# Optimization experiments

Hardware: AMD Instinct MI355X
Metric: run time of the kernel (lower is better)

Reference implementation:

```python
import jax, jax.numpy as jnp
import numpy as np

N, E, H, W, K = 16, 128, 128, 128, 8  # batch, num_experts, height, width, top-k


def setup_inputs() -> dict:
    key = jax.random.key(0)
    k1, k2, k3 = jax.random.split(key, 3)
    return {
        "x": jax.random.normal(k1, (N, E, H, W), dtype=jnp.float32),        # unused by forward math (kept for signature fidelity)
        "experts": jax.random.normal(k2, (N, E, H, W), dtype=jnp.float32),  # per-expert output maps
        "gate_w": jax.random.normal(k3, (E, E), dtype=jnp.float32) * 0.05,  # 1x1 gating projection (out, in)
        "gate_b": jnp.zeros((E,), dtype=jnp.float32),
    }


def reference(x, experts, gate_w, gate_b):
    # Gate: 1x1 conv over the expert-channel dim -> per-pixel routing logits, then softmax.
    logits = jnp.einsum('nehw,fe->nfhw', experts, gate_w) + gate_b[None, :, None, None]
    routing_weights = jax.nn.softmax(logits, axis=1)  # [N, E, H, W]

    # SMoERouting: per-pixel top-k expert selection, gather expert values, scale by gate weight.
    rw_t = jnp.transpose(routing_weights, (0, 2, 3, 1))       # [N, H, W, E]
    top_vals, top_idx = jax.lax.top_k(rw_t, K)                # [N, H, W, K]
    experts_t = jnp.transpose(experts, (0, 2, 3, 1))          # [N, H, W, E]
    gathered = jnp.take_along_axis(experts_t, top_idx, axis=-1)  # irregular gather [N, H, W, K]
    selected = gathered * top_vals
    return jnp.transpose(selected, (0, 3, 1, 2))              # [N, K, H, W]
```

## Files before the change

kernel.cpp:

```cpp
#include <hip/hip_runtime.h>
#include <math.h>

#define NB 16
#define NE 128
#define NK 8
#define HW 16384
#define NPIX (NB * HW)

__device__ float g_gwT[NE * NE];

__global__ __launch_bounds__(256) void cvt_gw_kernel(const float* __restrict__ gate_w) {
    int i = blockIdx.x * 256 + threadIdx.x;
    if (i < NE * NE) {
        int e = i >> 7;
        int f = i & 127;
        g_gwT[i] = gate_w[f * NE + e];
    }
}

__global__ __launch_bounds__(256) void moe_kernel(const float* __restrict__ experts,
                                                  const float* __restrict__ gate_b,
                                                  float* __restrict__ out) {
    const int p  = blockIdx.x * 256 + threadIdx.x;
    const int n  = p >> 14;
    const int hw = p & (HW - 1);

    const float* xp = experts + ((size_t)n * NE * HW + hw);

    float acc[NE];
#pragma unroll
    for (int f = 0; f < NE; ++f) acc[f] = 0.0f;

    for (int e = 0; e < NE; ++e) {
        float xe = xp[(size_t)e * HW];
        const float* gw = &g_gwT[e * NE];
#pragma unroll
        for (int f = 0; f < NE; ++f) {
            acc[f] = fmaf(gw[f], xe, acc[f]);
        }
    }

#pragma unroll
    for (int f = 0; f < NE; ++f) acc[f] = acc[f] + gate_b[f];

    float m = acc[0];
#pragma unroll
    for (int f = 1; f < NE; ++f) m = fmaxf(m, acc[f]);

#pragma unroll
    for (int f = 0; f < NE; ++f) {
        acc[f] = (float)exp((double)(acc[f] - m));
    }

    float s = acc[0];
#pragma unroll
    for (int f = 1; f < NE; ++f) s = s + acc[f];

#pragma unroll
    for (int f = 0; f < NE; ++f) acc[f] = acc[f] / s;

    float t_v[NK];
    int   t_i[NK];
#pragma unroll
    for (int i = 0; i < NK; ++i) { t_v[i] = -1.0f; t_i[i] = 0; }

#pragma unroll
    for (int f = 0; f < NE; ++f) {
        float v  = acc[f];
        int   ix = f;
#pragma unroll
        for (int i = 0; i < NK; ++i) {
            bool gt = v > t_v[i];
            float tv = t_v[i]; int ti = t_i[i];
            t_v[i] = gt ? v  : tv;
            t_i[i] = gt ? ix : ti;
            v      = gt ? tv : v;
            ix     = gt ? ti : ix;
        }
    }

    float* op = out + ((size_t)n * NK * HW + hw);
#pragma unroll
    for (int k = 0; k < NK; ++k) {
        float xv = xp[(size_t)t_i[k] * HW];
        op[(size_t)k * HW] = t_v[k] * xv;
    }
}

extern "C" void kernel_launch(void* const* d_in, const int* in_sizes, int n_in,
                              void* d_out, int out_size, void* d_ws, size_t ws_size,
                              hipStream_t stream) {
    const float* experts = (const float*)d_in[1];
    const float* gate_w  = (const float*)d_in[2];
    const float* gate_b  = (const float*)d_in[3];
    float* out = (float*)d_out;

    hipLaunchKernelGGL(cvt_gw_kernel, dim3((NE * NE + 255) / 256), dim3(256), 0, stream, gate_w);
    hipLaunchKernelGGL(moe_kernel, dim3(NPIX / 256), dim3(256), 0, stream, experts, gate_b, out);
}
```

Before: 287.2 us.

## Use packed FP32 FMA with scalar gate weights and prefetch expert loads

Replaces the scalar per-output FMA loop with v_pk_fma_f32 inline asm that takes two gate weights at a time from scalar registers, which halves the VALU instruction count of the 128x128 projection. Expert values are loaded four channels ahead to hide global memory latency, and launch bounds now request two blocks per CU. Inline asm with an "s" constraint relies on the weights being wave-uniform and may cost extra SGPR moves, and the occupancy hint could cause register spills.

```diff
diff --git a/kernel.cpp b/kernel.cpp
--- a/kernel.cpp
+++ b/kernel.cpp
@@ -6,6 +6,8 @@
 #define NK 8
 #define HW 16384
 #define NPIX (NB * HW)
+
+typedef float v2f __attribute__((ext_vector_type(2)));
 
 __device__ float g_gwT[NE * NE];
 
@@ -18,46 +20,86 @@
     }
 }
 
-__global__ __launch_bounds__(256) void moe_kernel(const float* __restrict__ experts,
-                                                  const float* __restrict__ gate_b,
-                                                  float* __restrict__ out) {
+#define E_STEP(EIDX, XV)                                                \
+    {                                                                   \
+        v2f xb; xb.x = (XV); xb.y = (XV);                               \
+        const v2f* g2 = (const v2f*)&g_gwT[(size_t)(EIDX) * NE];        \
+        _Pragma("unroll")                                               \
+        for (int j = 0; j < NE / 2; ++j) {                              \
+            asm("v_pk_fma_f32 %0, %2, %1, %0"                           \
+                : "+v"(acc[j])                                          \
+                : "v"(xb), "s"(g2[j]));                                 \
+        }                                                               \
+    }
+
+__global__ __launch_bounds__(256, 2) void moe_kernel(const float* __restrict__ experts,
+                                                     const float* __restrict__ gate_b,
+                                                     float* __restrict__ out) {
     const int p  = blockIdx.x * 256 + threadIdx.x;
     const int n  = p >> 14;
     const int hw = p & (HW - 1);
 
     const float* xp = experts + ((size_t)n * NE * HW + hw);
 
-    float acc[NE];
+    v2f acc[NE / 2];
 #pragma unroll
-    for (int f = 0; f < NE; ++f) acc[f] = 0.0f;
+    for (int j = 0; j < NE / 2; ++j) acc[j] = (v2f){0.0f, 0.0f};
 
-    for (int e = 0; e < NE; ++e) {
-        float xe = xp[(size_t)e * HW];
-        const float* gw = &g_gwT[e * NE];
+    float xc0 = xp[0 * (size_t)HW];
+    float xc1 = xp[1 * (size_t)HW];
+    float xc2 = xp[2 * (size_t)HW];
+    float xc3 = xp[3 * (size_t)HW];
+
+    int e = 0;
+    for (; e < NE - 4; e += 4) {
+        float nx0 = xp[(size_t)(e + 4) * HW];
+        float nx1 = xp[(size_t)(e + 5) * HW];
+        float nx2 = xp[(size_t)(e + 6) * HW];
+        float nx3 = xp[(size_t)(e + 7) * HW];
+        E_STEP(e + 0, xc0);
+        E_STEP(e + 1, xc1);
+        E_STEP(e + 2, xc2);
+        E_STEP(e + 3, xc3);
+        xc0 = nx0; xc1 = nx1; xc2 = nx2; xc3 = nx3;
+    }
+    E_STEP(e + 0, xc0);
+    E_STEP(e + 1, xc1);
+    E_STEP(e + 2, xc2);
+    E_STEP(e + 3, xc3);
+
 #pragma unroll
-        for (int f = 0; f < NE; ++f) {
-            acc[f] = fmaf(gw[f], xe, acc[f]);
-        }
+    for (int j = 0; j < NE / 2; ++j) {
+        acc[j].x = acc[j].x + gate_b[2 * j];
+        acc[j].y = acc[j].y + gate_b[2 * j + 1];
+    }
+
+    float m = acc[0].x;
+    m = fmaxf(m, acc[0].y);
+#pragma unroll
+    for (int j = 1; j < NE / 2; ++j) {
+        m = fmaxf(m, acc[j].x);
+        m = fmaxf(m, acc[j].y);
     }
 
 #pragma unroll
-    for (int f = 0; f < NE; ++f) acc[f] = acc[f] + gate_b[f];
+    for (int j = 0; j < NE / 2; ++j) {
+        acc[j].x = (float)exp((double)(acc[j].x - m));
+        acc[j].y = (float)exp((double)(acc[j].y - m));
+    }
 
-    float m = acc[0];
+    float s = acc[0].x;
+    s = s + acc[0].y;
 #pragma unroll
-    for (int f = 1; f < NE; ++f) m = fmaxf(m, acc[f]);
+    for (int j = 1; j < NE / 2; ++j) {
+        s = s + acc[j].x;
+        s = s + acc[j].y;
+    }
 
 #pragma unroll
-    for (int f = 0; f < NE; ++f) {
-        acc[f] = (float)exp((double)(acc[f] - m));
+    for (int j = 0; j < NE / 2; ++j) {
+        acc[j].x = acc[j].x / s;
+        acc[j].y = acc[j].y / s;
     }
-
-    float s = acc[0];
-#pragma unroll
-    for (int f = 1; f < NE; ++f) s = s + acc[f];
-
-#pragma unroll
-    for (int f = 0; f < NE; ++f) acc[f] = acc[f] / s;
 
     float t_v[NK];
     int   t_i[NK];
@@ -65,17 +107,20 @@
     for (int i = 0; i < NK; ++i) { t_v[i] = -1.0f; t_i[i] = 0; }
 
 #pragma unroll
-    for (int f = 0; f < NE; ++f) {
-        float v  = acc[f];
-        int   ix = f;
+    for (int j = 0; j < NE / 2; ++j) {
 #pragma unroll
-        for (int i = 0; i < NK; ++i) {
-            bool gt = v > t_v[i];
-            float tv = t_v[i]; int ti = t_i[i];
-            t_v[i] = gt ? v  : tv;
-            t_i[i] = gt ? ix : ti;
-            v      = gt ? tv : v;
-            ix     = gt ? ti : ix;
+        for (int h = 0; h < 2; ++h) {
+            float v  = h ? acc[j].y : acc[j].x;
+            int   ix = 2 * j + h;
+#pragma unroll
+            for (int i = 0; i < NK; ++i) {
+                bool gt = v > t_v[i];
+                float tv = t_v[i]; int ti = t_i[i];
+                t_v[i] = gt ? v  : tv;
+                t_i[i] = gt ? ix : ti;
+                v      = gt ? tv : v;
+                ix     = gt ? ti : ix;
+            }
         }
     }
 
```

Result: slower. 802.0 us (+179.2%).

## Double-buffer expert channel loads into LDS via async global_load_lds

Applied to the files above, without the earlier changes.

The expert values are now staged into shared memory in chunks of 16 channels using the direct global-to-LDS load builtin. A double buffer prefetches the next chunk while the current one feeds the per-pixel gate FMAs, with a barrier after each chunk. This aims to hide global load latency in the gating matmul loop. In exchange it adds 16 KB of LDS per block and a block-wide barrier per chunk. Synchronisation on the async loads relies only on __syncthreads and there is no explicit wait on the LDS-load counter.

```diff
diff --git a/kernel.cpp b/kernel.cpp
--- a/kernel.cpp
+++ b/kernel.cpp
@@ -6,6 +6,9 @@
 #define NK 8
 #define HW 16384
 #define NPIX (NB * HW)
+
+#define CH 16
+#define NCHUNK (NE / CH)
 
 __device__ float g_gwT[NE * NE];
 
@@ -21,24 +24,52 @@
 __global__ __launch_bounds__(256) void moe_kernel(const float* __restrict__ experts,
                                                   const float* __restrict__ gate_b,
                                                   float* __restrict__ out) {
-    const int p  = blockIdx.x * 256 + threadIdx.x;
-    const int n  = p >> 14;
-    const int hw = p & (HW - 1);
+    const int tid = threadIdx.x;
+    const int wv  = tid >> 6;
+    const int p   = blockIdx.x * 256 + tid;
+    const int n   = p >> 14;
+    const int hw  = p & (HW - 1);
 
-    const float* xp = experts + ((size_t)n * NE * HW + hw);
+    const float* xp    = experts + ((size_t)n * NE * HW + hw);
+    const float* xbase = experts + ((size_t)n * NE * HW + ((size_t)blockIdx.x * 256 & (HW - 1)));
+
+    __shared__ float xs[2][CH][256];
+
+#define STAGE(c, b)                                                                   \
+    {                                                                                 \
+        const float* gsrc = xbase + (size_t)(c) * CH * HW;                            \
+        _Pragma("unroll")                                                             \
+        for (int i = 0; i < CH; ++i) {                                                \
+            __builtin_amdgcn_global_load_lds(                                         \
+                (const __attribute__((address_space(1))) void*)(gsrc + (size_t)i * HW + tid), \
+                (__attribute__((address_space(3))) void*)&xs[b][i][wv * 64],          \
+                4, 0, 0);                                                             \
+        }                                                                             \
+    }
 
     float acc[NE];
 #pragma unroll
     for (int f = 0; f < NE; ++f) acc[f] = 0.0f;
 
-    for (int e = 0; e < NE; ++e) {
-        float xe = xp[(size_t)e * HW];
-        const float* gw = &g_gwT[e * NE];
+    STAGE(0, 0);
+    __syncthreads();
+
+    for (int c = 0; c < NCHUNK; ++c) {
+        const int cur = c & 1;
+        if (c + 1 < NCHUNK) STAGE(c + 1, cur ^ 1);
+
 #pragma unroll
-        for (int f = 0; f < NE; ++f) {
-            acc[f] = fmaf(gw[f], xe, acc[f]);
+        for (int i = 0; i < CH; ++i) {
+            float xe = xs[cur][i][tid];
+            const float* gw = &g_gwT[(size_t)(c * CH + i) * NE];
+#pragma unroll
+            for (int f = 0; f < NE; ++f) {
+                acc[f] = fmaf(gw[f], xe, acc[f]);
+            }
         }
+        __syncthreads();
     }
+#undef STAGE
 
 #pragma unroll
     for (int f = 0; f < NE; ++f) acc[f] = acc[f] + gate_b[f];
```

New measurement: 584.2 us. +103.4%, slower.

## Stage gate weights in LDS and prefetch expert inputs in groups of eight

Applied to the files above, without the earlier changes.

Each block copies the transposed 128x128 gate matrix into shared memory and then reads it with float4 broadcast loads instead of scalar global loads. The expert loads are software-pipelined: the next group of eight channel values is fetched while the current group is accumulated. This targets global-memory and scalar load latency in the gating matmul. It costs 64KB of LDS per block, which limits occupancy, adds extra registers on top of the 128 accumulators, and every block repeats the copy.

```diff
diff --git a/kernel.cpp b/kernel.cpp
--- a/kernel.cpp
+++ b/kernel.cpp
@@ -21,22 +21,55 @@
 __global__ __launch_bounds__(256) void moe_kernel(const float* __restrict__ experts,
                                                   const float* __restrict__ gate_b,
                                                   float* __restrict__ out) {
-    const int p  = blockIdx.x * 256 + threadIdx.x;
-    const int n  = p >> 14;
-    const int hw = p & (HW - 1);
+    const int tid = threadIdx.x;
+    const int p   = blockIdx.x * 256 + tid;
+    const int n   = p >> 14;
+    const int hw  = p & (HW - 1);
 
     const float* xp = experts + ((size_t)n * NE * HW + hw);
+
+    __shared__ __align__(16) float gws[NE * NE];
+    {
+        const float4* src = (const float4*)g_gwT;
+        float4* dst = (float4*)gws;
+#pragma unroll
+        for (int i = 0; i < 16; ++i) {
+            dst[tid + 256 * i] = src[tid + 256 * i];
+        }
+    }
+    __syncthreads();
 
     float acc[NE];
 #pragma unroll
     for (int f = 0; f < NE; ++f) acc[f] = 0.0f;
 
-    for (int e = 0; e < NE; ++e) {
-        float xe = xp[(size_t)e * HW];
-        const float* gw = &g_gwT[e * NE];
+    float xr[8];
 #pragma unroll
-        for (int f = 0; f < NE; ++f) {
-            acc[f] = fmaf(gw[f], xe, acc[f]);
+    for (int i = 0; i < 8; ++i) xr[i] = xp[(size_t)i * HW];
+
+    for (int eg = 0; eg < 16; ++eg) {
+        float xn[8];
+        if (eg < 15) {
+            const float* xq = xp + (size_t)(eg + 1) * 8 * HW;
+#pragma unroll
+            for (int i = 0; i < 8; ++i) xn[i] = xq[(size_t)i * HW];
+        }
+#pragma unroll
+        for (int i = 0; i < 8; ++i) {
+            const float xe = xr[i];
+            const float4* grow = (const float4*)&gws[(eg * 8 + i) * NE];
+#pragma unroll
+            for (int j = 0; j < NE / 4; ++j) {
+                float4 g = grow[j];
+                acc[4 * j + 0] = fmaf(g.x, xe, acc[4 * j + 0]);
+                acc[4 * j + 1] = fmaf(g.y, xe, acc[4 * j + 1]);
+                acc[4 * j + 2] = fmaf(g.z, xe, acc[4 * j + 2]);
+                acc[4 * j + 3] = fmaf(g.w, xe, acc[4 * j + 3]);
+            }
+        }
+        if (eg < 15) {
+#pragma unroll
+            for (int i = 0; i < 8; ++i) xr[i] = xn[i];
         }
     }
 
```

Measured after the change: 394.6 us. 1.37x slower.
